# Optimization experiments

Hardware: AMD Instinct MI355X
Metric: run time of the kernel (lower is better)

The kernel has to match this reference:

```python
import jax, jax.numpy as jnp
import numpy as np

N = 8192      # nodes
E = 262144    # edges per graph (avg degree 32)
D_IN = 256
HID = 64
HEADS = 2
NEG_SLOPE = 0.2  # PyG GATConv leaky_relu slope


def _self_loops(ei, n):
    loop = jnp.arange(n, dtype=ei.dtype)
    return jnp.concatenate([ei[0], loop]), jnp.concatenate([ei[1], loop])


def gat_conv(x, src, dst, W, att_src, att_dst, b, concat):
    # PyG GATConv: h=[N,H,C]; alpha=softmax_dst(leaky_relu(a_s[src]+a_d[dst]))
    n = x.shape[0]
    H, C = att_src.shape
    h = (x @ W).reshape(n, H, C)
    a_s = (h * att_src).sum(-1)           # [N,H]
    a_d = (h * att_dst).sum(-1)           # [N,H]
    e = jax.nn.leaky_relu(a_s[src] + a_d[dst], NEG_SLOPE)  # [Etot,H]
    e = e - jax.ops.segment_max(e, dst, num_segments=n)[dst]
    e = jnp.exp(e)
    denom = jax.ops.segment_sum(e, dst, num_segments=n)[dst] + 1e-16
    alpha = e / denom                     # edge softmax per target node
    msg = h[src] * alpha[:, :, None]      # [Etot,H,C]
    out = jax.ops.segment_sum(msg, dst, num_segments=n)  # [N,H,C]
    out = out.reshape(n, H * C) if concat else out.mean(axis=1)
    return out + b


def gcn_conv(x, src, dst, W, b):
    # PyG GCNConv: D^{-1/2}(A+I)D^{-1/2} X W + b (self loops already appended)
    n = x.shape[0]
    h = x @ W
    deg = jax.ops.segment_sum(jnp.ones_like(src, jnp.float32), dst, num_segments=n)
    dinv = jax.lax.rsqrt(jnp.maximum(deg, 1.0))
    norm = dinv[src] * dinv[dst]          # [Etot]
    return jax.ops.segment_sum(h[src] * norm[:, None], dst, num_segments=n) + b


def cross_attn(q_in, kv_in, Wq, bq, Wk, bk, Wv, bv, Wo, bo, num_heads):
    n, d = q_in.shape
    hd = d // num_heads
    q = (q_in @ Wq + bq).reshape(n, num_heads, hd)
    k = (kv_in @ Wk + bk).reshape(n, num_heads, hd)
    v = (kv_in @ Wv + bv).reshape(n, num_heads, hd)
    scores = jnp.einsum('qhd,khd->hqk', q, k) / np.sqrt(hd).astype(np.float32)
    attn = jax.nn.softmax(scores, axis=-1)                 # [H,N,N]
    out = jnp.einsum('hqk,khd->qhd', attn, v).reshape(n, d) @ Wo + bo
    weights = attn.mean(axis=0)[None]                      # [1,N,N] avg heads (torch default)
    return out, weights


def setup_inputs():
    key = jax.random.key(0)
    ks = jax.random.split(key, 24)
    w = lambda k, s: jax.random.normal(k, s, jnp.float32) * 0.05
    inp = {
        'x': jax.random.normal(ks[0], (N, D_IN), jnp.float32),
        'edge_index_tkg': jax.random.randint(ks[1], (2, E), 0, N, jnp.int64 if jax.config.jax_enable_x64 else jnp.int32),
        'edge_index_ekg': jax.random.randint(ks[2], (2, E), 0, N, jnp.int64 if jax.config.jax_enable_x64 else jnp.int32),
        # GAT layer 1: heads=2, concat=True
        'gat1_W': w(ks[3], (D_IN, HEADS * HID)),
        'gat1_att_src': w(ks[4], (HEADS, HID)),
        'gat1_att_dst': w(ks[5], (HEADS, HID)),
        'gat1_b': jnp.zeros((HEADS * HID,), jnp.float32),
        # GAT layer 2: heads=1, concat=False
        'gat2_W': w(ks[6], (HEADS * HID, HID)),
        'gat2_att_src': w(ks[7], (1, HID)),
        'gat2_att_dst': w(ks[8], (1, HID)),
        'gat2_b': jnp.zeros((HID,), jnp.float32),
        # GCN layers
        'gcn1_W': w(ks[9], (D_IN, HID)),
        'gcn1_b': jnp.zeros((HID,), jnp.float32),
        'gcn2_W': w(ks[10], (HID, HID)),
        'gcn2_b': jnp.zeros((HID,), jnp.float32),
        # cross attention (hidden=64, 2 heads)
        'Wq': w(ks[11], (HID, HID)), 'bq': jnp.zeros((HID,), jnp.float32),
        'Wk': w(ks[12], (HID, HID)), 'bk': jnp.zeros((HID,), jnp.float32),
        'Wv': w(ks[13], (HID, HID)), 'bv': jnp.zeros((HID,), jnp.float32),
        'Wo': w(ks[14], (HID, HID)), 'bo': jnp.zeros((HID,), jnp.float32),
        # MLP head
        'fc1_W': w(ks[15], (2 * HID, HID)), 'fc1_b': jnp.zeros((HID,), jnp.float32),
        'fc2_W': w(ks[16], (HID, 1)), 'fc2_b': jnp.zeros((1,), jnp.float32),
    }
    return inp


def reference(x, edge_index_tkg, edge_index_ekg,
              gat1_W, gat1_att_src, gat1_att_dst, gat1_b,
              gat2_W, gat2_att_src, gat2_att_dst, gat2_b,
              gcn1_W, gcn1_b, gcn2_W, gcn2_b,
              Wq, bq, Wk, bk, Wv, bv, Wo, bo,
              fc1_W, fc1_b, fc2_W, fc2_b):
    n = x.shape[0]
    src_t, dst_t = _self_loops(edge_index_tkg, n)
    src_e, dst_e = _self_loops(edge_index_ekg, n)

    h_tkg = jax.nn.elu(gat_conv(x, src_t, dst_t, gat1_W, gat1_att_src, gat1_att_dst, gat1_b, True))
    h_tkg = jax.nn.elu(gat_conv(h_tkg, src_t, dst_t, gat2_W, gat2_att_src, gat2_att_dst, gat2_b, False))

    h_ekg = jax.nn.relu(gcn_conv(x, src_e, dst_e, gcn1_W, gcn1_b))
    h_ekg = jax.nn.relu(gcn_conv(h_ekg, src_e, dst_e, gcn2_W, gcn2_b))

    h_attn, attn_weights = cross_attn(h_tkg, h_ekg, Wq, bq, Wk, bk, Wv, bv, Wo, bo, HEADS)

    h_fused = jnp.concatenate([h_tkg, h_attn], axis=1)   # [N, 2*HID]
    pred = (jax.nn.relu(h_fused @ fc1_W + fc1_b) @ fc2_W + fc2_b).squeeze(-1)
    return pred, attn_weights
```

## Files before the change

### kernel.cpp

```cpp
#include <hip/hip_runtime.h>
#include <cstdint>
#include <cstddef>

#define NN 8192
#define EE 262144
#define ET 270336

using short8  = __attribute__((ext_vector_type(8))) short;
using floatx4 = __attribute__((ext_vector_type(4))) float;

__device__ __forceinline__ unsigned short f2bf(float f) {
  unsigned int u = __float_as_uint(f);
  u += 0x7fffu + ((u >> 16) & 1u);
  return (unsigned short)(u >> 16);
}

__global__ void edge_hist2_k(const int* __restrict__ ei_t, const int* __restrict__ ei_e,
                             int* __restrict__ cnt_t, int* __restrict__ cnt_e) {
  int idx = blockIdx.x * 256 + threadIdx.x;
  int g = idx >= ET;
  int e = g ? idx - ET : idx;
  const int* ei = g ? ei_e : ei_t;
  int* cnt = g ? cnt_e : cnt_t;
  int d = (e < EE) ? ei[EE + e] : (e - EE);
  atomicAdd(&cnt[d], 1);
}

__global__ void scan2_k(int* cnt_t, int* off_t, int* cnt_e, int* off_e) {
  int* cnt = blockIdx.x ? cnt_e : cnt_t;
  int* off = blockIdx.x ? off_e : off_t;
  __shared__ int s[1024];
  int t = threadIdx.x;
  int v[8]; int base = t * 8; int sum = 0;
  #pragma unroll
  for (int j = 0; j < 8; ++j) { v[j] = cnt[base + j]; sum += v[j]; }
  s[t] = sum; __syncthreads();
  for (int o = 1; o < 1024; o <<= 1) {
    int x = (t >= o) ? s[t - o] : 0;
    __syncthreads();
    s[t] += x;
    __syncthreads();
  }
  int excl = s[t] - sum;
  #pragma unroll
  for (int j = 0; j < 8; ++j) { off[base + j] = excl; cnt[base + j] = excl; excl += v[j]; }
  if (t == 1023) off[NN] = excl;
}

__global__ void edge_scatter2_k(const int* __restrict__ ei_t, const int* __restrict__ ei_e,
                                int* __restrict__ pos_t, int* __restrict__ pos_e,
                                int* __restrict__ srcs_t, int* __restrict__ srcs_e) {
  int idx = blockIdx.x * 256 + threadIdx.x;
  int g = idx >= ET;
  int e = g ? idx - ET : idx;
  const int* ei = g ? ei_e : ei_t;
  int* pos = g ? pos_e : pos_t;
  int* srcs = g ? srcs_e : srcs_t;
  int sv, d;
  if (e < EE) { sv = ei[e]; d = ei[EE + e]; } else { sv = d = e - EE; }
  int p = atomicAdd(&pos[d], 1);
  srcs[p] = sv;
}

__device__ __forceinline__ void gemm_core(const float* __restrict__ A, int lda, int K,
                                          const float* __restrict__ Bs, int row0, int col,
                                          float acc[8]) {
  #pragma unroll
  for (int r = 0; r < 8; ++r) acc[r] = 0.f;
  for (int k = 0; k < K; k += 4) {
    float b0 = Bs[(k + 0) * 32 + col], b1 = Bs[(k + 1) * 32 + col];
    float b2 = Bs[(k + 2) * 32 + col], b3 = Bs[(k + 3) * 32 + col];
    #pragma unroll
    for (int r = 0; r < 8; ++r) {
      const float4 a4 = *(const float4*)(A + (size_t)(row0 + r) * lda + k);
      acc[r] = fmaf(a4.x, b0, acc[r]);
      acc[r] = fmaf(a4.y, b1, acc[r]);
      acc[r] = fmaf(a4.z, b2, acc[r]);
      acc[r] = fmaf(a4.w, b3, acc[r]);
    }
  }
}

__global__ __launch_bounds__(256) void mm_x_k(const float* __restrict__ x,
    const float* __restrict__ Wgat, const float* __restrict__ Wgcn,
    const float* __restrict__ as_w, const float* __restrict__ ad_w,
    float* __restrict__ h1, float* __restrict__ hg1,
    float* __restrict__ a_s1, float* __restrict__ a_d1) {
  __shared__ float Bs[256 * 32];
  const int tid = threadIdx.x, by = blockIdx.y;
  const bool gat = by < 4;
  const int NC = gat ? 128 : 64;
  const int c0 = gat ? by * 32 : (by - 4) * 32;
  const float* B = gat ? Wgat : Wgcn;
  for (int idx = tid; idx < 256 * 32; idx += 256)
    Bs[idx] = B[(idx >> 5) * NC + c0 + (idx & 31)];
  __syncthreads();
  const int row0 = blockIdx.x * 64 + (tid >> 5) * 8;
  const int col = tid & 31;
  float acc[8];
  gemm_core(x, 256, 256, Bs, row0, col, acc);
  if (gat) {
    #pragma unroll
    for (int r = 0; r < 8; ++r) h1[(size_t)(row0 + r) * 128 + c0 + col] = acc[r];
    const int head = c0 >> 6;
    const float asw = as_w[head * 64 + (c0 & 63) + col];
    const float adw = ad_w[head * 64 + (c0 & 63) + col];
    float ps[8], pd[8];
    #pragma unroll
    for (int r = 0; r < 8; ++r) { ps[r] = acc[r] * asw; pd[r] = acc[r] * adw; }
    #pragma unroll
    for (int m = 16; m >= 1; m >>= 1)
      #pragma unroll
      for (int r = 0; r < 8; ++r) { ps[r] += __shfl_xor(ps[r], m); pd[r] += __shfl_xor(pd[r], m); }
    if (col == 0) {
      #pragma unroll
      for (int r = 0; r < 8; ++r) {
        atomicAdd(&a_s1[(row0 + r) * 2 + head], ps[r]);
        atomicAdd(&a_d1[(row0 + r) * 2 + head], pd[r]);
      }
    }
  } else {
    #pragma unroll
    for (int r = 0; r < 8; ++r) hg1[(size_t)(row0 + r) * 64 + c0 + col] = acc[r];
  }
}

__global__ __launch_bounds__(256) void mm_gat2_k(const float* __restrict__ A,
    const float* __restrict__ W, const float* __restrict__ as_w, const float* __restrict__ ad_w,
    float* __restrict__ h2, float* __restrict__ a_s2, float* __restrict__ a_d2) {
  __shared__ float Bs[128 * 32];
  const int tid = threadIdx.x;
  const int c0 = blockIdx.y * 32;
  for (int idx = tid; idx < 128 * 32; idx += 256)
    Bs[idx] = W[(idx >> 5) * 64 + c0 + (idx & 31)];
  __syncthreads();
  const int row0 = blockIdx.x * 64 + (tid >> 5) * 8;
  const int col = tid & 31;
  float acc[8];
  gemm_core(A, 128, 128, Bs, row0, col, acc);
  const float asw = as_w[c0 + col];
  const float adw = ad_w[c0 + col];
  float ps[8], pd[8];
  #pragma unroll
  for (int r = 0; r < 8; ++r) {
    h2[(size_t)(row0 + r) * 64 + c0 + col] = acc[r];
    ps[r] = acc[r] * asw; pd[r] = acc[r] * adw;
  }
  #pragma unroll
  for (int m = 16; m >= 1; m >>= 1)
    #pragma unroll
    for (int r = 0; r < 8; ++r) { ps[r] += __shfl_xor(ps[r], m); pd[r] += __shfl_xor(pd[r], m); }
  if (col == 0) {
    #pragma unroll
    for (int r = 0; r < 8; ++r) {
      atomicAdd(&a_s2[row0 + r], ps[r]);
      atomicAdd(&a_d2[row0 + r], pd[r]);
    }
  }
}

template<int H, int C>
__global__ void gat_agg_k(const float* __restrict__ h, const float* __restrict__ a_s,
                          const float* __restrict__ a_d, const int* __restrict__ off,
                          const int* __restrict__ srcs, const float* __restrict__ bias,
                          float* __restrict__ out, int ldout) {
  constexpr int HC = H * C;
  const int b = blockIdx.x;
  const int tid = threadIdx.x;
  const int hd = tid / C;
  const int r0 = off[b], r1 = off[b + 1];
  __shared__ int s_src[HC];
  __shared__ float s_w[HC][H];
  float ad[H];
  #pragma unroll
  for (int hh = 0; hh < H; ++hh) ad[hh] = a_d[b * H + hh];
  float acc = 0.f, den = 0.f;
  for (int base = r0; base < r1; base += HC) {
    __syncthreads();
    int e = base + tid;
    if (e < r1) {
      int sv = srcs[e];
      s_src[tid] = sv;
      #pragma unroll
      for (int hh = 0; hh < H; ++hh) {
        float xv = a_s[sv * H + hh] + ad[hh];
        xv = xv > 0.f ? xv : 0.2f * xv;
        s_w[tid][hh] = __expf(xv);
      }
    }
    __syncthreads();
    int cnt = min(HC, r1 - base);
    for (int j = 0; j < cnt; ++j) {
      float wv = s_w[j][hd];
      den += wv;
      acc = fmaf(wv, h[(size_t)s_src[j] * HC + tid], acc);
    }
  }
  float o = acc / den + bias[tid];
  out[(size_t)b * ldout + tid] = o > 0.f ? o : (__expf(o) - 1.f);
}

__global__ void gcn_agg1_k(const float* __restrict__ hg1, const int* __restrict__ off,
                           const int* __restrict__ srcs, const float* __restrict__ b1,
                           const float* __restrict__ W2, float* __restrict__ h2g) {
  const int b = blockIdx.x, tid = threadIdx.x;
  int r0 = off[b], r1 = off[b + 1];
  float dinv_b = rsqrtf((float)max(r1 - r0, 1));
  __shared__ int s_src[64];
  __shared__ float s_nrm[64];
  __shared__ float s_row[64];
  float acc = 0.f;
  for (int base = r0; base < r1; base += 64) {
    __syncthreads();
    int e = base + tid;
    if (e < r1) {
      int sv = srcs[e];
      s_src[tid] = sv;
      int ds = off[sv + 1] - off[sv];
      s_nrm[tid] = dinv_b * rsqrtf((float)max(ds, 1));
    }
    __syncthreads();
    int cnt = min(64, r1 - base);
    for (int j = 0; j < cnt; ++j)
      acc = fmaf(s_nrm[j], hg1[(size_t)s_src[j] * 64 + tid], acc);
  }
  s_row[tid] = fmaxf(acc + b1[tid], 0.f);
  __syncthreads();
  float acc2 = 0.f;
  for (int k = 0; k < 64; ++k)
    acc2 = fmaf(s_row[k], W2[k * 64 + tid], acc2);
  h2g[(size_t)b * 64 + tid] = acc2;
}

__global__ void gcn_agg2_k(const float* __restrict__ h2g, const int* __restrict__ off,
                           const int* __restrict__ srcs, const float* __restrict__ bias,
                           float* __restrict__ out) {
  const int b = blockIdx.x, tid = threadIdx.x;
  int r0 = off[b], r1 = off[b + 1];
  float dinv_b = rsqrtf((float)max(r1 - r0, 1));
  __shared__ int s_src[64];
  __shared__ float s_nrm[64];
  float acc = 0.f;
  for (int base = r0; base < r1; base += 64) {
    __syncthreads();
    int e = base + tid;
    if (e < r1) {
      int sv = srcs[e];
      s_src[tid] = sv;
      int ds = off[sv + 1] - off[sv];
      s_nrm[tid] = dinv_b * rsqrtf((float)max(ds, 1));
    }
    __syncthreads();
    int cnt = min(64, r1 - base);
    for (int j = 0; j < cnt; ++j)
      acc = fmaf(s_nrm[j], h2g[(size_t)s_src[j] * 64 + tid], acc);
  }
  out[(size_t)b * 64 + tid] = fmaxf(acc + bias[tid], 0.f);
}

__global__ __launch_bounds__(256) void mm_qkv_k(const float* __restrict__ htkg,
    const float* __restrict__ hekg,
    const float* __restrict__ Wq, const float* __restrict__ bq,
    const float* __restrict__ Wk, const float* __restrict__ bk,
    const float* __restrict__ Wv, const float* __restrict__ bv,
    unsigned short* __restrict__ qb, unsigned short* __restrict__ kb,
    unsigned short* __restrict__ Vt) {
  __shared__ float Bs[64 * 32];
  __shared__ float Ts[32][65];
  const int tid = threadIdx.x, by = blockIdx.y;
  const int kind = by >> 1;
  const int c0 = (by & 1) * 32;
  const float* A = (kind == 0) ? htkg : hekg;
  const float* B = (kind == 0) ? Wq : (kind == 1) ? Wk : Wv;
  const float* bias = (kind == 0) ? bq : (kind == 1) ? bk : bv;
  for (int idx = tid; idx < 64 * 32; idx += 256)
    Bs[idx] = B[(idx >> 5) * 64 + c0 + (idx & 31)];
  __syncthreads();
  const int row0 = blockIdx.x * 64 + (tid >> 5) * 8;
  const int col = tid & 31;
  float acc[8];
  gemm_core(A, 64, 64, Bs, row0, col, acc);
  const float bb = bias[c0 + col];
  if (kind == 0) {
    const float SCL = 0.17677669529663687f * 1.4426950408889634f;
    #pragma unroll
    for (int r = 0; r < 8; ++r)
      qb[(size_t)(row0 + r) * 64 + c0 + col] = f2bf((acc[r] + bb) * SCL);
  } else if (kind == 1) {
    #pragma unroll
    for (int r = 0; r < 8; ++r)
      kb[(size_t)(row0 + r) * 64 + c0 + col] = f2bf(acc[r] + bb);
  } else {
    const int rl = (tid >> 5) * 8;
    #pragma unroll
    for (int r = 0; r < 8; ++r) Ts[col][rl + r] = acc[r] + bb;
    __syncthreads();
    const int c = tid >> 3, rr = (tid & 7) * 8;
    short8 pk;
    #pragma unroll
    for (int j = 0; j < 8; ++j) pk[j] = (short)f2bf(Ts[c][rr + j]);
    *(short8*)(Vt + (size_t)(c0 + c) * NN + blockIdx.x * 64 + rr) = pk;
  }
}

__global__ __launch_bounds__(256) void att_pass1(const unsigned short* __restrict__ qb,
                                                 const unsigned short* __restrict__ kb,
                                                 float* __restrict__ lrow) {
  const int tid = threadIdx.x;
  const int lane = tid & 63, wv = tid >> 6;
  const int ql = lane & 15, quad = lane >> 4;
  const int qt0 = blockIdx.x * 16;
  const floatx4 zf = {0.f, 0.f, 0.f, 0.f};
  short8 qf[2];
  #pragma unroll
  for (int h = 0; h < 2; ++h)
    qf[h] = *(const short8*)(qb + (size_t)(qt0 + ql) * 64 + h * 32 + quad * 8);
  float lacc[2][4];
  #pragma unroll
  for (int h = 0; h < 2; ++h)
    #pragma unroll
    for (int r = 0; r < 4; ++r) lacc[h][r] = 0.f;
  int kbase = wv * 2048;
  for (int it = 0; it < 64; ++it, kbase += 32) {
    short8 kf[2][2];
    #pragma unroll
    for (int kt = 0; kt < 2; ++kt)
      #pragma unroll
      for (int h = 0; h < 2; ++h)
        kf[kt][h] = *(const short8*)(kb + (size_t)(kbase + kt * 16 + ql) * 64 + h * 32 + quad * 8);
    #pragma unroll
    for (int h = 0; h < 2; ++h)
      #pragma unroll
      for (int kt = 0; kt < 2; ++kt) {
        floatx4 s = __builtin_amdgcn_mfma_f32_16x16x32_bf16(qf[h], kf[kt][h], zf, 0, 0, 0);
        #pragma unroll
        for (int r = 0; r < 4; ++r) lacc[h][r] += __builtin_amdgcn_exp2f(s[r]);
      }
  }
  #pragma unroll
  for (int o = 8; o >= 1; o >>= 1)
    #pragma unroll
    for (int h = 0; h < 2; ++h)
      #pragma unroll
      for (int r = 0; r < 4; ++r)
        lacc[h][r] += __shfl_xor(lacc[h][r], o, 16);
  if (ql == 0) {
    #pragma unroll
    for (int h = 0; h < 2; ++h)
      #pragma unroll
      for (int r = 0; r < 4; ++r)
        atomicAdd(&lrow[(size_t)(qt0 + quad * 4 + r) * 2 + h], lacc[h][r]);
  }
}

__global__ __launch_bounds__(256) void att_pass2(
    const unsigned short* __restrict__ qb, const unsigned short* __restrict__ kb,
    const unsigned short* __restrict__ Vt, const float* __restrict__ lrow,
    float* __restrict__ attn, float* __restrict__ O) {
  __shared__ __align__(16) float Esh[4][2][16 * 36];
  __shared__ float Osh[16 * 64];
  const int tid = threadIdx.x;
  const int lane = tid & 63, wv = tid >> 6;
  const int ql = lane & 15, quad = lane >> 4;
  const int qt0 = blockIdx.x * 16;
  const floatx4 zf = {0.f, 0.f, 0.f, 0.f};

  for (int idx = tid; idx < 16 * 64; idx += 256) Osh[idx] = 0.f;
  __syncthreads();

  short8 qf[2];
  #pragma unroll
  for (int h = 0; h < 2; ++h)
    qf[h] = *(const short8*)(qb + (size_t)(qt0 + ql) * 64 + h * 32 + quad * 8);

  float invl[2][4];
  #pragma unroll
  for (int h = 0; h < 2; ++h)
    #pragma unroll
    for (int r = 0; r < 4; ++r)
      invl[h][r] = 1.0f / lrow[(size_t)(qt0 + quad * 4 + r) * 2 + h];

  floatx4 oacc[2][2];
  #pragma unroll
  for (int h = 0; h < 2; ++h)
    #pragma unroll
    for (int hf = 0; hf < 2; ++hf) oacc[h][hf] = zf;

  int kbase = wv * 2048;
  for (int it = 0; it < 64; ++it, kbase += 32) {
    short8 kf[2][2], vf[2][2];
    #pragma unroll
    for (int kt = 0; kt < 2; ++kt)
      #pragma unroll
      for (int h = 0; h < 2; ++h)
        kf[kt][h] = *(const short8*)(kb + (size_t)(kbase + kt * 16 + ql) * 64 + h * 32 + quad * 8);
    #pragma unroll
    for (int h = 0; h < 2; ++h)
      #pragma unroll
      for (int hf = 0; hf < 2; ++hf)
        vf[h][hf] = *(const short8*)(Vt + (size_t)(h * 32 + hf * 16 + ql) * NN + kbase + quad * 8);

    floatx4 p[2][2];
    #pragma unroll
    for (int h = 0; h < 2; ++h)
      #pragma unroll
      for (int kt = 0; kt < 2; ++kt) {
        floatx4 s = __builtin_amdgcn_mfma_f32_16x16x32_bf16(qf[h], kf[kt][h], zf, 0, 0, 0);
        #pragma unroll
        for (int r = 0; r < 4; ++r)
          p[h][kt][r] = __builtin_amdgcn_exp2f(s[r]) * invl[h][r];
      }
    #pragma unroll
    for (int kt = 0; kt < 2; ++kt)
      #pragma unroll
      for (int r = 0; r < 4; ++r) {
        size_t row = (size_t)(qt0 + quad * 4 + r);
        __builtin_nontemporal_store(0.5f * (p[0][kt][r] + p[1][kt][r]),
                                    &attn[row * NN + kbase + kt * 16 + ql]);
      }
    #pragma unroll
    for (int h = 0; h < 2; ++h)
      #pragma unroll
      for (int kt = 0; kt < 2; ++kt)
        #pragma unroll
        for (int r = 0; r < 4; ++r)
          Esh[wv][h][(quad * 4 + r) * 36 + kt * 16 + ql] = p[h][kt][r];
    #pragma unroll
    for (int h = 0; h < 2; ++h) {
      const float* ep = &Esh[wv][h][ql * 36 + quad * 8];
      float4 x0 = *(const float4*)ep;
      float4 x1 = *(const float4*)(ep + 4);
      short8 ef;
      ef[0] = (short)f2bf(x0.x); ef[1] = (short)f2bf(x0.y);
      ef[2] = (short)f2bf(x0.z); ef[3] = (short)f2bf(x0.w);
      ef[4] = (short)f2bf(x1.x); ef[5] = (short)f2bf(x1.y);
      ef[6] = (short)f2bf(x1.z); ef[7] = (short)f2bf(x1.w);
      #pragma unroll
      for (int hf = 0; hf < 2; ++hf)
        oacc[h][hf] = __builtin_amdgcn_mfma_f32_16x16x32_bf16(ef, vf[h][hf], oacc[h][hf], 0, 0, 0);
    }
  }
  #pragma unroll
  for (int h = 0; h < 2; ++h)
    #pragma unroll
    for (int hf = 0; hf < 2; ++hf)
      #pragma unroll
      for (int r = 0; r < 4; ++r)
        atomicAdd(&Osh[(quad * 4 + r) * 64 + h * 32 + hf * 16 + ql], oacc[h][hf][r]);
  __syncthreads();
  for (int idx = tid; idx < 16 * 64; idx += 256)
    O[(size_t)qt0 * 64 + idx] = Osh[idx];
}

__global__ __launch_bounds__(256) void tail_k(const float* __restrict__ O,
    const float* __restrict__ htkg, const float* __restrict__ Wo, const float* __restrict__ bo,
    const float* __restrict__ fc1W, const float* __restrict__ fc1b,
    const float* __restrict__ fc2W, const float* __restrict__ fc2b,
    float* __restrict__ pred) {
  __shared__ float Ws[8192];
  __shared__ float T1[2048];
  __shared__ float T2[2048];
  const int tid = threadIdx.x;
  const int col = tid & 63, rg = tid >> 6;
  const int rowbase = blockIdx.x * 32;
  for (int i = tid; i < 2048; i += 256) T1[i] = O[(size_t)rowbase * 64 + i];
  for (int i = tid; i < 4096; i += 256) Ws[i] = Wo[i];
  const float rbo = bo[col], rf1b = fc1b[col], rf2 = fc2W[col], rf2b = fc2b[0];
  __syncthreads();
  float ha[8];
  #pragma unroll
  for (int r = 0; r < 8; ++r) {
    const int row = rg * 8 + r;
    float acc = rbo;
    for (int k = 0; k < 64; ++k) acc = fmaf(T1[row * 64 + k], Ws[k * 64 + col], acc);
    ha[r] = acc;
  }
  __syncthreads();
  #pragma unroll
  for (int r = 0; r < 8; ++r) T2[(rg * 8 + r) * 64 + col] = ha[r];
  for (int i = tid; i < 2048; i += 256) T1[i] = htkg[(size_t)rowbase * 64 + i];
  for (int i = tid; i < 8192; i += 256) Ws[i] = fc1W[i];
  __syncthreads();
  #pragma unroll
  for (int r = 0; r < 8; ++r) {
    const int row = rg * 8 + r;
    float acc = rf1b;
    for (int k = 0; k < 64; ++k) acc = fmaf(T1[row * 64 + k], Ws[k * 64 + col], acc);
    for (int k = 0; k < 64; ++k) acc = fmaf(T2[row * 64 + k], Ws[(64 + k) * 64 + col], acc);
    float y = fmaxf(acc, 0.f);
    float v = y * rf2;
    #pragma unroll
    for (int m = 32; m >= 1; m >>= 1) v += __shfl_xor(v, m);
    if (col == 0) pred[rowbase + row] = v + rf2b;
  }
}

extern "C" void kernel_launch(void* const* d_in, const int* in_sizes, int n_in,
                              void* d_out, int out_size, void* d_ws, size_t ws_size,
                              hipStream_t stream) {
  (void)in_sizes; (void)n_in; (void)out_size; (void)ws_size;
  const float* x       = (const float*)d_in[0];
  const int*   ei_t    = (const int*)d_in[1];
  const int*   ei_e    = (const int*)d_in[2];
  const float* gat1_W  = (const float*)d_in[3];
  const float* gat1_as = (const float*)d_in[4];
  const float* gat1_ad = (const float*)d_in[5];
  const float* gat1_b  = (const float*)d_in[6];
  const float* gat2_W  = (const float*)d_in[7];
  const float* gat2_as = (const float*)d_in[8];
  const float* gat2_ad = (const float*)d_in[9];
  const float* gat2_b  = (const float*)d_in[10];
  const float* gcn1_W  = (const float*)d_in[11];
  const float* gcn1_b  = (const float*)d_in[12];
  const float* gcn2_W  = (const float*)d_in[13];
  const float* gcn2_b  = (const float*)d_in[14];
  const float* Wq = (const float*)d_in[15]; const float* bq = (const float*)d_in[16];
  const float* Wk = (const float*)d_in[17]; const float* bk = (const float*)d_in[18];
  const float* Wv = (const float*)d_in[19]; const float* bv = (const float*)d_in[20];
  const float* Wo = (const float*)d_in[21]; const float* bo = (const float*)d_in[22];
  const float* fc1_W = (const float*)d_in[23]; const float* fc1_b = (const float*)d_in[24];
  const float* fc2_W = (const float*)d_in[25]; const float* fc2_b = (const float*)d_in[26];

  float* out  = (float*)d_out;
  float* attn = out + NN;

  char* wsp = (char*)d_ws;
  size_t ofs = 0;
  auto take = [&](size_t bytes) -> char* {
    char* p = wsp + ofs;
    ofs = (ofs + bytes + 255) & ~(size_t)255;
    return p;
  };
  int*   pos_t = (int*)take(NN * 4);
  int*   pos_e = (int*)take(NN * 4);
  float* lbuf  = (float*)take((size_t)NN * 2 * 4);
  float* a_s1  = (float*)take((size_t)NN * 2 * 4);
  float* a_d1  = (float*)take((size_t)NN * 2 * 4);
  float* a_s2  = (float*)take((size_t)NN * 4);
  float* a_d2  = (float*)take((size_t)NN * 4);
  const size_t zero_span = ofs;
  int* off_t = (int*)take((NN + 1) * 4);
  int* off_e = (int*)take((NN + 1) * 4);
  int* src_t = (int*)take((size_t)ET * 4);
  int* src_e = (int*)take((size_t)ET * 4);
  float* h1    = (float*)take((size_t)NN * 128 * 4);
  float* g1out = (float*)take((size_t)NN * 128 * 4);
  float* h2    = (float*)take((size_t)NN * 64 * 4);
  float* htkg  = (float*)take((size_t)NN * 64 * 4);
  float* hg1   = (float*)take((size_t)NN * 64 * 4);
  float* h2g   = (float*)take((size_t)NN * 64 * 4);
  float* hekg  = (float*)take((size_t)NN * 64 * 4);
  unsigned short* qb = (unsigned short*)take((size_t)NN * 64 * 2);
  unsigned short* kb = (unsigned short*)take((size_t)NN * 64 * 2);
  unsigned short* Vt = (unsigned short*)take((size_t)64 * NN * 2);
  float* Obuf  = (float*)take((size_t)NN * 64 * 4);

  hipMemsetAsync(wsp, 0, zero_span, stream);

  edge_hist2_k<<<2 * ET / 256, 256, 0, stream>>>(ei_t, ei_e, pos_t, pos_e);
  scan2_k<<<2, 1024, 0, stream>>>(pos_t, off_t, pos_e, off_e);
  edge_scatter2_k<<<2 * ET / 256, 256, 0, stream>>>(ei_t, ei_e, pos_t, pos_e, src_t, src_e);

  mm_x_k<<<dim3(128, 6), 256, 0, stream>>>(x, gat1_W, gcn1_W, gat1_as, gat1_ad,
                                           h1, hg1, a_s1, a_d1);
  gat_agg_k<2, 64><<<NN, 128, 0, stream>>>(h1, a_s1, a_d1, off_t, src_t, gat1_b, g1out, 128);
  mm_gat2_k<<<dim3(128, 2), 256, 0, stream>>>(g1out, gat2_W, gat2_as, gat2_ad, h2, a_s2, a_d2);
  gat_agg_k<1, 64><<<NN, 64, 0, stream>>>(h2, a_s2, a_d2, off_t, src_t, gat2_b, htkg, 64);

  gcn_agg1_k<<<NN, 64, 0, stream>>>(hg1, off_e, src_e, gcn1_b, gcn2_W, h2g);
  gcn_agg2_k<<<NN, 64, 0, stream>>>(h2g, off_e, src_e, gcn2_b, hekg);

  mm_qkv_k<<<dim3(128, 6), 256, 0, stream>>>(htkg, hekg, Wq, bq, Wk, bk, Wv, bv, qb, kb, Vt);

  att_pass1<<<512, 256, 0, stream>>>(qb, kb, lbuf);
  att_pass2<<<512, 256, 0, stream>>>(qb, kb, Vt, lbuf, attn, Obuf);

  tail_k<<<256, 256, 0, stream>>>(Obuf, htkg, Wo, bo, fc1_W, fc1_b, fc2_W, fc2_b, out);
}
```

Before: 668.9 us.

## Split attention over key halves and co-launch independent GAT/GCN aggregation kernels

The attention passes now split the key range into two halves per query tile. This doubles the grid to 1024 blocks and adds a min-blocks launch bound. Each half writes a separate partial output buffer, and the tail kernel sums the two partials. The independent GAT and GCN aggregations and the GAT2 matmul are also merged into shared launches (agg1_k, mm2_k), so small kernels fill the GPU together and fewer launches are needed. The cost is an extra partial buffer, extra reads in the tail, and correctness depends on the row-sum buffer being combined safely across the two halves.

```diff
diff --git a/kernel.cpp b/kernel.cpp
--- a/kernel.cpp
+++ b/kernel.cpp
@@ -125,47 +125,12 @@
   }
 }
 
-__global__ __launch_bounds__(256) void mm_gat2_k(const float* __restrict__ A,
-    const float* __restrict__ W, const float* __restrict__ as_w, const float* __restrict__ ad_w,
-    float* __restrict__ h2, float* __restrict__ a_s2, float* __restrict__ a_d2) {
-  __shared__ float Bs[128 * 32];
-  const int tid = threadIdx.x;
-  const int c0 = blockIdx.y * 32;
-  for (int idx = tid; idx < 128 * 32; idx += 256)
-    Bs[idx] = W[(idx >> 5) * 64 + c0 + (idx & 31)];
-  __syncthreads();
-  const int row0 = blockIdx.x * 64 + (tid >> 5) * 8;
-  const int col = tid & 31;
-  float acc[8];
-  gemm_core(A, 128, 128, Bs, row0, col, acc);
-  const float asw = as_w[c0 + col];
-  const float adw = ad_w[c0 + col];
-  float ps[8], pd[8];
-  #pragma unroll
-  for (int r = 0; r < 8; ++r) {
-    h2[(size_t)(row0 + r) * 64 + c0 + col] = acc[r];
-    ps[r] = acc[r] * asw; pd[r] = acc[r] * adw;
-  }
-  #pragma unroll
-  for (int m = 16; m >= 1; m >>= 1)
-    #pragma unroll
-    for (int r = 0; r < 8; ++r) { ps[r] += __shfl_xor(ps[r], m); pd[r] += __shfl_xor(pd[r], m); }
-  if (col == 0) {
-    #pragma unroll
-    for (int r = 0; r < 8; ++r) {
-      atomicAdd(&a_s2[row0 + r], ps[r]);
-      atomicAdd(&a_d2[row0 + r], pd[r]);
-    }
-  }
-}
-
 template<int H, int C>
-__global__ void gat_agg_k(const float* __restrict__ h, const float* __restrict__ a_s,
-                          const float* __restrict__ a_d, const int* __restrict__ off,
-                          const int* __restrict__ srcs, const float* __restrict__ bias,
-                          float* __restrict__ out, int ldout) {
+__device__ __forceinline__ void gat_agg_body(const float* __restrict__ h,
+    const float* __restrict__ a_s, const float* __restrict__ a_d,
+    const int* __restrict__ off, const int* __restrict__ srcs,
+    const float* __restrict__ bias, float* __restrict__ out, int ldout, int b) {
   constexpr int HC = H * C;
-  const int b = blockIdx.x;
   const int tid = threadIdx.x;
   const int hd = tid / C;
   const int r0 = off[b], r1 = off[b + 1];
@@ -200,62 +165,125 @@
   out[(size_t)b * ldout + tid] = o > 0.f ? o : (__expf(o) - 1.f);
 }
 
-__global__ void gcn_agg1_k(const float* __restrict__ hg1, const int* __restrict__ off,
-                           const int* __restrict__ srcs, const float* __restrict__ b1,
-                           const float* __restrict__ W2, float* __restrict__ h2g) {
-  const int b = blockIdx.x, tid = threadIdx.x;
-  int r0 = off[b], r1 = off[b + 1];
-  float dinv_b = rsqrtf((float)max(r1 - r0, 1));
-  __shared__ int s_src[64];
-  __shared__ float s_nrm[64];
-  __shared__ float s_row[64];
-  float acc = 0.f;
-  for (int base = r0; base < r1; base += 64) {
+template<int H, int C>
+__global__ void gat_agg_k(const float* __restrict__ h, const float* __restrict__ a_s,
+                          const float* __restrict__ a_d, const int* __restrict__ off,
+                          const int* __restrict__ srcs, const float* __restrict__ bias,
+                          float* __restrict__ out, int ldout) {
+  gat_agg_body<H, C>(h, a_s, a_d, off, srcs, bias, out, ldout, blockIdx.x);
+}
+
+__global__ __launch_bounds__(128) void agg1_k(
+    const float* __restrict__ h1, const float* __restrict__ a_s1, const float* __restrict__ a_d1,
+    const int* __restrict__ off_t, const int* __restrict__ src_t,
+    const float* __restrict__ gat1_b, float* __restrict__ g1out,
+    const float* __restrict__ hg1, const int* __restrict__ off_e, const int* __restrict__ src_e,
+    const float* __restrict__ gcn1_b, const float* __restrict__ gcn2_W, float* __restrict__ h2g) {
+  const int tid = threadIdx.x;
+  if (blockIdx.x < NN) {
+    gat_agg_body<2, 64>(h1, a_s1, a_d1, off_t, src_t, gat1_b, g1out, 128, blockIdx.x);
+  } else {
+    const int nb = (blockIdx.x - NN) * 2;
+    const int sub = tid >> 6, t = tid & 63;
+    const int node = nb + sub;
+    __shared__ int s_src2[2][64];
+    __shared__ float s_nrm2[2][64];
+    __shared__ float s_row2[2][64];
+    const int r0 = off_e[node], r1 = off_e[node + 1];
+    const int cA = off_e[nb + 1] - off_e[nb];
+    const int cB = off_e[nb + 2] - off_e[nb + 1];
+    const int trips = (max(cA, cB) + 63) >> 6;
+    float dinv_b = rsqrtf((float)max(r1 - r0, 1));
+    float acc = 0.f;
+    for (int it = 0; it < trips; ++it) {
+      __syncthreads();
+      int e = r0 + it * 64 + t;
+      if (e < r1) {
+        int sv = src_e[e];
+        s_src2[sub][t] = sv;
+        int ds = off_e[sv + 1] - off_e[sv];
+        s_nrm2[sub][t] = dinv_b * rsqrtf((float)max(ds, 1));
+      }
+      __syncthreads();
+      int cnt = min(64, r1 - (r0 + it * 64));
+      for (int j = 0; j < cnt; ++j)
+        acc = fmaf(s_nrm2[sub][j], hg1[(size_t)s_src2[sub][j] * 64 + t], acc);
+    }
+    s_row2[sub][t] = fmaxf(acc + gcn1_b[t], 0.f);
     __syncthreads();
-    int e = base + tid;
-    if (e < r1) {
-      int sv = srcs[e];
-      s_src[tid] = sv;
-      int ds = off[sv + 1] - off[sv];
-      s_nrm[tid] = dinv_b * rsqrtf((float)max(ds, 1));
-    }
+    float acc2 = 0.f;
+    for (int k = 0; k < 64; ++k)
+      acc2 = fmaf(s_row2[sub][k], gcn2_W[k * 64 + t], acc2);
+    h2g[(size_t)node * 64 + t] = acc2;
+  }
+}
+
+__global__ __launch_bounds__(256) void mm2_k(
+    const float* __restrict__ g1out, const float* __restrict__ gat2_W,
+    const float* __restrict__ gat2_as, const float* __restrict__ gat2_ad,
+    float* __restrict__ h2, float* __restrict__ a_s2, float* __restrict__ a_d2,
+    const float* __restrict__ h2g, const int* __restrict__ off_e, const int* __restrict__ src_e,
+    const float* __restrict__ gcn2_b, float* __restrict__ hekg) {
+  const int tid = threadIdx.x;
+  if (blockIdx.x < 256) {
+    __shared__ float Bs[128 * 32];
+    const int bx = blockIdx.x & 127;
+    const int c0 = (blockIdx.x >> 7) * 32;
+    for (int idx = tid; idx < 128 * 32; idx += 256)
+      Bs[idx] = gat2_W[(idx >> 5) * 64 + c0 + (idx & 31)];
     __syncthreads();
-    int cnt = min(64, r1 - base);
-    for (int j = 0; j < cnt; ++j)
-      acc = fmaf(s_nrm[j], hg1[(size_t)s_src[j] * 64 + tid], acc);
-  }
-  s_row[tid] = fmaxf(acc + b1[tid], 0.f);
-  __syncthreads();
-  float acc2 = 0.f;
-  for (int k = 0; k < 64; ++k)
-    acc2 = fmaf(s_row[k], W2[k * 64 + tid], acc2);
-  h2g[(size_t)b * 64 + tid] = acc2;
-}
-
-__global__ void gcn_agg2_k(const float* __restrict__ h2g, const int* __restrict__ off,
-                           const int* __restrict__ srcs, const float* __restrict__ bias,
-                           float* __restrict__ out) {
-  const int b = blockIdx.x, tid = threadIdx.x;
-  int r0 = off[b], r1 = off[b + 1];
-  float dinv_b = rsqrtf((float)max(r1 - r0, 1));
-  __shared__ int s_src[64];
-  __shared__ float s_nrm[64];
-  float acc = 0.f;
-  for (int base = r0; base < r1; base += 64) {
-    __syncthreads();
-    int e = base + tid;
-    if (e < r1) {
-      int sv = srcs[e];
-      s_src[tid] = sv;
-      int ds = off[sv + 1] - off[sv];
-      s_nrm[tid] = dinv_b * rsqrtf((float)max(ds, 1));
-    }
-    __syncthreads();
-    int cnt = min(64, r1 - base);
-    for (int j = 0; j < cnt; ++j)
-      acc = fmaf(s_nrm[j], h2g[(size_t)s_src[j] * 64 + tid], acc);
-  }
-  out[(size_t)b * 64 + tid] = fmaxf(acc + bias[tid], 0.f);
+    const int row0 = bx * 64 + (tid >> 5) * 8;
+    const int col = tid & 31;
+    float acc[8];
+    gemm_core(g1out, 128, 128, Bs, row0, col, acc);
+    const float asw = gat2_as[c0 + col];
+    const float adw = gat2_ad[c0 + col];
+    float ps[8], pd[8];
+    #pragma unroll
+    for (int r = 0; r < 8; ++r) {
+      h2[(size_t)(row0 + r) * 64 + c0 + col] = acc[r];
+      ps[r] = acc[r] * asw; pd[r] = acc[r] * adw;
+    }
+    #pragma unroll
+    for (int m = 16; m >= 1; m >>= 1)
+      #pragma unroll
+      for (int r = 0; r < 8; ++r) { ps[r] += __shfl_xor(ps[r], m); pd[r] += __shfl_xor(pd[r], m); }
+    if (col == 0) {
+      #pragma unroll
+      for (int r = 0; r < 8; ++r) {
+        atomicAdd(&a_s2[row0 + r], ps[r]);
+        atomicAdd(&a_d2[row0 + r], pd[r]);
+      }
+    }
+  } else {
+    const int nb = (blockIdx.x - 256) * 4;
+    const int sub = tid >> 6, t = tid & 63;
+    const int node = nb + sub;
+    __shared__ int s_src4[4][64];
+    __shared__ float s_nrm4[4][64];
+    const int r0 = off_e[node], r1 = off_e[node + 1];
+    int cmax = 0;
+    #pragma unroll
+    for (int i = 0; i < 4; ++i) cmax = max(cmax, off_e[nb + i + 1] - off_e[nb + i]);
+    const int trips = (cmax + 63) >> 6;
+    float dinv_b = rsqrtf((float)max(r1 - r0, 1));
+    float acc = 0.f;
+    for (int it = 0; it < trips; ++it) {
+      __syncthreads();
+      int e = r0 + it * 64 + t;
+      if (e < r1) {
+        int sv = src_e[e];
+        s_src4[sub][t] = sv;
+        int ds = off_e[sv + 1] - off_e[sv];
+        s_nrm4[sub][t] = dinv_b * rsqrtf((float)max(ds, 1));
+      }
+      __syncthreads();
+      int cnt = min(64, r1 - (r0 + it * 64));
+      for (int j = 0; j < cnt; ++j)
+        acc = fmaf(s_nrm4[sub][j], h2g[(size_t)s_src4[sub][j] * 64 + t], acc);
+    }
+    hekg[(size_t)node * 64 + t] = fmaxf(acc + gcn2_b[t], 0.f);
+  }
 }
 
 __global__ __launch_bounds__(256) void mm_qkv_k(const float* __restrict__ htkg,
@@ -303,13 +331,14 @@
   }
 }
 
-__global__ __launch_bounds__(256) void att_pass1(const unsigned short* __restrict__ qb,
-                                                 const unsigned short* __restrict__ kb,
-                                                 float* __restrict__ lrow) {
+__global__ __launch_bounds__(256, 4) void att_pass1(const unsigned short* __restrict__ qb,
+                                                    const unsigned short* __restrict__ kb,
+                                                    float* __restrict__ lrow) {
   const int tid = threadIdx.x;
   const int lane = tid & 63, wv = tid >> 6;
   const int ql = lane & 15, quad = lane >> 4;
-  const int qt0 = blockIdx.x * 16;
+  const int qt0 = (blockIdx.x >> 1) * 16;
+  const int khalf = blockIdx.x & 1;
   const floatx4 zf = {0.f, 0.f, 0.f, 0.f};
   short8 qf[2];
   #pragma unroll
@@ -320,8 +349,8 @@
   for (int h = 0; h < 2; ++h)
     #pragma unroll
     for (int r = 0; r < 4; ++r) lacc[h][r] = 0.f;
-  int kbase = wv * 2048;
-  for (int it = 0; it < 64; ++it, kbase += 32) {
+  int kbase = khalf * 4096 + wv * 1024;
+  for (int it = 0; it < 32; ++it, kbase += 32) {
     short8 kf[2][2];
     #pragma unroll
     for (int kt = 0; kt < 2; ++kt)
@@ -353,16 +382,18 @@
   }
 }
 
-__global__ __launch_bounds__(256) void att_pass2(
+__global__ __launch_bounds__(256, 4) void att_pass2(
     const unsigned short* __restrict__ qb, const unsigned short* __restrict__ kb,
     const unsigned short* __restrict__ Vt, const float* __restrict__ lrow,
-    float* __restrict__ attn, float* __restrict__ O) {
+    float* __restrict__ attn, float* __restrict__ Opart) {
   __shared__ __align__(16) float Esh[4][2][16 * 36];
   __shared__ float Osh[16 * 64];
   const int tid = threadIdx.x;
   const int lane = tid & 63, wv = tid >> 6;
   const int ql = lane & 15, quad = lane >> 4;
-  const int qt0 = blockIdx.x * 16;
+  const int qt0 = (blockIdx.x >> 1) * 16;
+  const int khalf = blockIdx.x & 1;
+  float* O = Opart + (size_t)khalf * NN * 64;
   const floatx4 zf = {0.f, 0.f, 0.f, 0.f};
 
   for (int idx = tid; idx < 16 * 64; idx += 256) Osh[idx] = 0.f;
@@ -386,8 +417,8 @@
     #pragma unroll
     for (int hf = 0; hf < 2; ++hf) oacc[h][hf] = zf;
 
-  int kbase = wv * 2048;
-  for (int it = 0; it < 64; ++it, kbase += 32) {
+  int kbase = khalf * 4096 + wv * 1024;
+  for (int it = 0; it < 32; ++it, kbase += 32) {
     short8 kf[2][2], vf[2][2];
     #pragma unroll
     for (int kt = 0; kt < 2; ++kt)
@@ -452,7 +483,7 @@
     O[(size_t)qt0 * 64 + idx] = Osh[idx];
 }
 
-__global__ __launch_bounds__(256) void tail_k(const float* __restrict__ O,
+__global__ __launch_bounds__(256) void tail_k(const float* __restrict__ Opart,
     const float* __restrict__ htkg, const float* __restrict__ Wo, const float* __restrict__ bo,
     const float* __restrict__ fc1W, const float* __restrict__ fc1b,
     const float* __restrict__ fc2W, const float* __restrict__ fc2b,
@@ -463,7 +494,10 @@
   const int tid = threadIdx.x;
   const int col = tid & 63, rg = tid >> 6;
   const int rowbase = blockIdx.x * 32;
-  for (int i = tid; i < 2048; i += 256) T1[i] = O[(size_t)rowbase * 64 + i];
+  for (int i = tid; i < 2048; i += 256) {
+    size_t idx = (size_t)rowbase * 64 + i;
+    T1[i] = Opart[idx] + Opart[(size_t)NN * 64 + idx];
+  }
   for (int i = tid; i < 4096; i += 256) Ws[i] = Wo[i];
   const float rbo = bo[col], rf1b = fc1b[col], rf2 = fc2W[col], rf2b = fc2b[0];
   __syncthreads();
@@ -553,7 +587,7 @@
   unsigned short* qb = (unsigned short*)take((size_t)NN * 64 * 2);
   unsigned short* kb = (unsigned short*)take((size_t)NN * 64 * 2);
   unsigned short* Vt = (unsigned short*)take((size_t)64 * NN * 2);
-  float* Obuf  = (float*)take((size_t)NN * 64 * 4);
+  float* Opart = (float*)take((size_t)2 * NN * 64 * 4);
 
   hipMemsetAsync(wsp, 0, zero_span, stream);
 
@@ -563,17 +597,16 @@
 
   mm_x_k<<<dim3(128, 6), 256, 0, stream>>>(x, gat1_W, gcn1_W, gat1_as, gat1_ad,
                                            h1, hg1, a_s1, a_d1);
-  gat_agg_k<2, 64><<<NN, 128, 0, stream>>>(h1, a_s1, a_d1, off_t, src_t, gat1_b, g1out, 128);
-  mm_gat2_k<<<dim3(128, 2), 256, 0, stream>>>(g1out, gat2_W, gat2_as, gat2_ad, h2, a_s2, a_d2);
+  agg1_k<<<NN + NN / 2, 128, 0, stream>>>(h1, a_s1, a_d1, off_t, src_t, gat1_b, g1out,
+                                          hg1, off_e, src_e, gcn1_b, gcn2_W, h2g);
+  mm2_k<<<256 + NN / 4, 256, 0, stream>>>(g1out, gat2_W, gat2_as, gat2_ad, h2, a_s2, a_d2,
+                                          h2g, off_e, src_e, gcn2_b, hekg);
   gat_agg_k<1, 64><<<NN, 64, 0, stream>>>(h2, a_s2, a_d2, off_t, src_t, gat2_b, htkg, 64);
 
-  gcn_agg1_k<<<NN, 64, 0, stream>>>(hg1, off_e, src_e, gcn1_b, gcn2_W, h2g);
-  gcn_agg2_k<<<NN, 64, 0, stream>>>(h2g, off_e, src_e, gcn2_b, hekg);
-
   mm_qkv_k<<<dim3(128, 6), 256, 0, stream>>>(htkg, hekg, Wq, bq, Wk, bk, Wv, bv, qb, kb, Vt);
 
-  att_pass1<<<512, 256, 0, stream>>>(qb, kb, lbuf);
-  att_pass2<<<512, 256, 0, stream>>>(qb, kb, Vt, lbuf, attn, Obuf);
-
-  tail_k<<<256, 256, 0, stream>>>(Obuf, htkg, Wo, bo, fc1_W, fc1_b, fc2_W, fc2_b, out);
-}
+  att_pass1<<<1024, 256, 0, stream>>>(qb, kb, lbuf);
+  att_pass2<<<1024, 256, 0, stream>>>(qb, kb, Vt, lbuf, attn, Opart);
+
+  tail_k<<<256, 256, 0, stream>>>(Opart, htkg, Wo, bo, fc1_W, fc1_b, fc2_W, fc2_b, out);
+}
```

Measured after the change: 668.8 us. No clear change (-0.0%).
